# Optimization experiments

Measured on AMD Instinct MI355X. Metric: run time of the kernel, lower is better.

The kernel has to match this reference:

```python
import jax, jax.numpy as jnp
import numpy as np
import math

SUN = 9.0            # global SuN constant in the repo (sudoku N=9)
TB = 16              # t-block size for L1-score computation (bounds peak memory)


def quick_gelu(x):
    return x * jax.nn.sigmoid(1.702 * x)


def l1_scores(q, k):
    # q, k: (b, t, h, d)  ->  scores (b, h, t, s) = -sum_d |q[b,t,h,:] - k[b,s,h,:]|
    # Blocked over t so we never materialize the full (b,t,s,h,d) tensor.
    b, t, h, d = q.shape
    nb = t // TB
    qb = q.reshape(b, nb, TB, h, d).swapaxes(0, 1)  # (nb, b, TB, h, d)

    def blk(carry, qi):
        # qi: (b, TB, h, d); diff block: (b, TB, s, h, d) -> (b, TB, s, h)
        s = -jnp.sum(jnp.abs(qi[:, :, None, :, :] - k[:, None, :, :, :]), axis=-1)
        return carry, s

    _, out = jax.lax.scan(blk, None, qb)            # (nb, b, TB, s, h)
    out = out.transpose(1, 0, 2, 3, 4).reshape(b, t, t, h)  # (b, t, s, h)
    return out.transpose(0, 3, 1, 2)                # (b, h, t, s)


def setup_inputs() -> dict:
    key = jax.random.key(0)
    ks = jax.random.split(key, 5)
    b, t, d, h = 8, 512, 128, 8
    x = jax.random.normal(ks[0], (b, t, d), dtype=jnp.float32)
    msk = jax.random.uniform(ks[1], (1, h, t, t), dtype=jnp.float32)
    # LinearM(d_model, n_head*2*d_model): w is (outdim, indim+1), uniform*scl, bias col zeroed
    scl_qv = math.sqrt(6.0) / math.sqrt(d + h * 2 * d)
    wqv_w = jax.random.uniform(ks[2], (h * 2 * d, d + 1), dtype=jnp.float32) * scl_qv
    wqv_w = wqv_w.at[:, -1].set(0.0)
    # LinearNobias(d_model, n_head): w is (n_head, d_model); used directly as per-head k-gate
    scl_k = math.sqrt(6.0) / math.sqrt(d + h)
    wk_w = jax.random.uniform(ks[3], (h, d), dtype=jnp.float32) * scl_k
    # fanout = LinearM(d_model, d_model)
    scl_f = math.sqrt(6.0) / math.sqrt(2 * d)
    fanout_w = jax.random.uniform(ks[4], (d, d + 1), dtype=jnp.float32) * scl_f
    fanout_w = fanout_w.at[:, -1].set(0.0)
    return {"x": x, "msk": msk, "wqv_w": wqv_w, "wk_w": wk_w, "fanout_w": fanout_w}


def reference(x, msk, wqv_w, wk_w, fanout_w):
    b, t, d = x.shape
    h = wk_w.shape[0]
    # wqv: LinearM -> (b, t, h*2*d)
    y = jnp.einsum('oi,bti->bto', wqv_w[:, :-1], x) + wqv_w[:, -1]
    y = y.reshape(b, t, h, 2 * d)
    q, v = y[..., :d], y[..., d:]                      # each (b, t, h, d)
    # k = x expanded per head, gated elementwise by wk.w (per-head, per-dim gate)
    k = x[:, :, None, :] * wk_w[None, None, :, :]      # (b, t, h, d)
    # gv gate: all heads enabled (init_zeros=False) -> identity multiply on v
    a = l1_scores(q, k) / math.sqrt(d)                 # (b, h, t, s)
    a = jax.nn.softmax(a, axis=3) * msk                # mask AFTER softmax (as in source)
    # combine + sum over heads: einsum('bhts,bshd->bthd') then sum(dim=2 of bthd == h)
    bo = jnp.einsum('bhts,bshd->btd', a, v)            # (b, t, d)
    yo = quick_gelu(bo + SUN / 2.0) - SUN / 2.0
    yo = jnp.einsum('oi,bti->bto', fanout_w[:, :-1], yo) + fanout_w[:, -1]
    return x + yo
```

## Files before the change

### kernel.cpp

```cpp
#include <hip/hip_runtime.h>
#include <hip/hip_bf16.h>
#include <math.h>

#define BB 8
#define TT 512
#define DD 128
#define HH 8
#define OO 2048
#define WCOLS 129
#define SCALE 0.08838834764831845f
#define IT 16
#define SC2 64
#define NC (TT / SC2)
#define Q8SCL 32.0f
#define Q8OFF 128.0f
#define SCALE_Q8 (SCALE / Q8SCL)

typedef __attribute__((ext_vector_type(8))) short short8;
typedef __attribute__((ext_vector_type(4))) float floatx4;

static __device__ __forceinline__ float bf2f(__hip_bfloat16 v) { return __bfloat162float(v); }
static __device__ __forceinline__ float us2f(unsigned short u) {
  union { unsigned int i; float f; } cv; cv.i = ((unsigned int)u) << 16; return cv.f;
}
static __device__ __forceinline__ unsigned short f2us(float f) {
  union { float f; unsigned int i; } cv; cv.f = f;
  unsigned int lsb = (cv.i >> 16) & 1u;
  return (unsigned short)((cv.i + 0x7fffu + lsb) >> 16);
}
static __device__ __forceinline__ float ldin(const void* p, int i, int isf) {
  return isf ? ((const float*)p)[i] : bf2f(((const __hip_bfloat16*)p)[i]);
}
static __device__ __forceinline__ unsigned char quant8(float v) {
  float f = fminf(fmaxf(v * Q8SCL + Q8OFF, 0.0f), 255.0f);
  return (unsigned char)(f + 0.5f);
}
static __device__ __forceinline__ int detect_isf(const void* x) {
  const unsigned int* w = (const unsigned int*)x;
  int cnt = 0;
#pragma unroll
  for (int i = 0; i < 64; ++i) {
    float a = fabsf(us2f((unsigned short)(w[i] & 0xFFFFu)));
    cnt += (a > 0.05f && a < 8.0f) ? 1 : 0;
  }
  return (cnt < 32) ? 1 : 0;
}

#if __has_builtin(__builtin_amdgcn_sad_u8)
#define SAD8(a, b, c) __builtin_amdgcn_sad_u8((a), (b), (c))
#elif __has_builtin(__builtin_amdgcn_sad_u16)
static __device__ __forceinline__ unsigned int SAD8(unsigned int a, unsigned int b, unsigned int c) {
  unsigned int alo = a & 0x00FF00FFu, ahi = (a >> 8) & 0x00FF00FFu;
  unsigned int blo = b & 0x00FF00FFu, bhi = (b >> 8) & 0x00FF00FFu;
  c = __builtin_amdgcn_sad_u16(alo, blo, c);
  return __builtin_amdgcn_sad_u16(ahi, bhi, c);
}
#else
static __device__ __forceinline__ unsigned int SAD8(unsigned int a, unsigned int b, unsigned int c) {
#pragma unroll
  for (int i = 0; i < 4; ++i) {
    int d = (int)((a >> (8 * i)) & 0xFF) - (int)((b >> (8 * i)) & 0xFF);
    c += (unsigned int)(d < 0 ? -d : d);
  }
  return c;
}
#endif

__global__ void k_prep(const void* __restrict__ x,
                       const void* __restrict__ wqv,
                       const void* __restrict__ wk,
                       const void* __restrict__ fo,
                       float* __restrict__ qvb,
                       float* __restrict__ foT, float* __restrict__ fob,
                       float* __restrict__ wkf,
                       unsigned short* __restrict__ wqvb,
                       unsigned short* __restrict__ xb,
                       int* __restrict__ flg) {
  int isf = detect_isf(x);
  int stride = gridDim.x * blockDim.x;
  int idx = blockIdx.x * blockDim.x + threadIdx.x;
  if (idx == 0) *flg = isf;
  for (int i = idx; i < OO * DD; i += stride) {
    int o = i >> 7, ii = i & 127;
    wqvb[i] = f2us(ldin(wqv, o * WCOLS + ii, isf));
  }
  for (int o = idx; o < OO; o += stride) qvb[o] = ldin(wqv, o * WCOLS + DD, isf);
  for (int i = idx; i < DD * DD; i += stride) {
    int o = i & (DD - 1), ii = i >> 7;
    foT[i] = ldin(fo, o * WCOLS + ii, isf);
  }
  for (int o = idx; o < DD; o += stride) fob[o] = ldin(fo, o * WCOLS + DD, isf);
  for (int i = idx; i < HH * DD; i += stride) wkf[i] = ldin(wk, i, isf);
  {
    int n4 = BB * TT * DD / 4;
    for (int i4 = idx; i4 < n4; i4 += stride) {
      if (isf) {
        float4 f = ((const float4*)x)[i4];
        unsigned int lo = (unsigned int)f2us(f.x) | ((unsigned int)f2us(f.y) << 16);
        unsigned int hi = (unsigned int)f2us(f.z) | ((unsigned int)f2us(f.w) << 16);
        uint2 o2; o2.x = lo; o2.y = hi;
        ((uint2*)xb)[i4] = o2;
      } else {
        ((uint2*)xb)[i4] = ((const uint2*)x)[i4];
      }
    }
  }
}

__global__ __launch_bounds__(256) void k_qvm(const unsigned short* __restrict__ xb,
                                             const unsigned short* __restrict__ wqvb,
                                             const float* __restrict__ qvb,
                                             unsigned char* __restrict__ q2b,
                                             unsigned short* __restrict__ vt) {
  __shared__ __align__(16) unsigned short xs[32][136];
  __shared__ __align__(16) unsigned short vtile[128][40];
  __shared__ __align__(16) unsigned char qtile[32][144];
  int rb = blockIdx.x * 32;
  int cb = blockIdx.y * 256;
  int tid = threadIdx.x;
#pragma unroll
  for (int p = 0; p < 2; ++p) {
    int e = tid + p * 256;
    int row = e >> 4, c16 = e & 15;
    *(uint4*)&xs[row][c16 * 8] = *(const uint4*)&xb[(size_t)(rb + row) * DD + c16 * 8];
  }
  __syncthreads();
  int lane = tid & 63;
  int w = tid >> 6;
  int mI = lane & 15;
  int quad = lane >> 4;
  int cw = cb + w * 64;
  floatx4 acc[2][4];
#pragma unroll
  for (int rt = 0; rt < 2; ++rt)
#pragma unroll
    for (int ct = 0; ct < 4; ++ct) acc[rt][ct] = (floatx4){0.f, 0.f, 0.f, 0.f};
#pragma unroll
  for (int j = 0; j < 4; ++j) {
    short8 av[2], bv[4];
#pragma unroll
    for (int rt = 0; rt < 2; ++rt)
      av[rt] = *(const short8*)&xs[rt * 16 + mI][j * 32 + quad * 8];
#pragma unroll
    for (int ct = 0; ct < 4; ++ct)
      bv[ct] = *(const short8*)&wqvb[(size_t)(cw + ct * 16 + mI) * DD + j * 32 + quad * 8];
#pragma unroll
    for (int rt = 0; rt < 2; ++rt)
#pragma unroll
      for (int ct = 0; ct < 4; ++ct)
        acc[rt][ct] = __builtin_amdgcn_mfma_f32_16x16x32_bf16(av[rt], bv[ct], acc[rt][ct], 0, 0, 0);
  }
#pragma unroll
  for (int rt = 0; rt < 2; ++rt) {
#pragma unroll
    for (int ct = 0; ct < 4; ++ct) {
      int o = cw + ct * 16 + mI;
      float bias = qvb[o];
      int cc = o & 255;
#pragma unroll
      for (int reg = 0; reg < 4; ++reg) {
        int r = rb + rt * 16 + quad * 4 + reg;
        float val = acc[rt][ct][reg] + bias;
        if (cc < DD) qtile[r - rb][cc] = quant8(val);
        else         vtile[cc - DD][r - rb] = f2us(val);
      }
    }
  }
  __syncthreads();
  {
    int b = rb >> 9, t0 = rb & 511;
    int h = cb >> 8;
    {
      int row = tid >> 3, c16 = (tid & 7) * 16;
      unsigned char* qdst = q2b + ((size_t)(b * HH + h) * TT + t0 + row) * DD + c16;
      *(uint4*)qdst = *(const uint4*)&qtile[row][c16];
    }
    {
      int n = tid >> 1, half = tid & 1;
      unsigned short* dst = vt + (((size_t)(b * HH + h) * DD) + n) * TT + t0 + half * 16;
      uint4 a0 = *(const uint4*)&vtile[n][half * 16];
      uint4 a1 = *(const uint4*)&vtile[n][half * 16 + 8];
      *(uint4*)&dst[0] = a0;
      *(uint4*)&dst[8] = a1;
    }
  }
}

__global__ void k_k(const unsigned short* __restrict__ xb,
                    const float* __restrict__ wkf, unsigned char* __restrict__ ku8) {
  int idx = blockIdx.x * 256 + threadIdx.x;
  int d = idx & 127;
  int s = (idx >> 7) & 511;
  int h = (idx >> 16) & 7;
  int b = idx >> 19;
  float val = us2f(xb[(b * TT + s) * DD + d]) * wkf[h * DD + d];
  ku8[idx] = quant8(val);
}

static __device__ __forceinline__ void sad_chunk(const unsigned int (*__restrict__ kb)[36],
                                                 const unsigned int (*__restrict__ qp)[36],
                                                 int r0, int r1, int si, int rot,
                                                 float* __restrict__ r, int c) {
  unsigned int a00 = 0, a01 = 0, a10 = 0, a11 = 0;
  const unsigned int* k0r = &kb[2 * si][0];
  const unsigned int* k1r = &kb[2 * si + 1][0];
  const unsigned int* q0r = &qp[r0][0];
  const unsigned int* q1r = &qp[r1][0];
#pragma unroll
  for (int j8 = 0; j8 < 32; j8 += 8) {
    int i0 = (j8 + rot) & 31;
    int i1 = (j8 + rot + 4) & 31;
    uint4 qa0 = *(const uint4*)&q0r[i0];
    uint4 qa1 = *(const uint4*)&q0r[i1];
    uint4 qb0 = *(const uint4*)&q1r[i0];
    uint4 qb1 = *(const uint4*)&q1r[i1];
    uint4 ka0 = *(const uint4*)&k0r[i0];
    uint4 ka1 = *(const uint4*)&k0r[i1];
    uint4 kb0 = *(const uint4*)&k1r[i0];
    uint4 kb1 = *(const uint4*)&k1r[i1];
    a00 = SAD8(qa0.x, ka0.x, a00); a00 = SAD8(qa0.y, ka0.y, a00);
    a00 = SAD8(qa0.z, ka0.z, a00); a00 = SAD8(qa0.w, ka0.w, a00);
    a00 = SAD8(qa1.x, ka1.x, a00); a00 = SAD8(qa1.y, ka1.y, a00);
    a00 = SAD8(qa1.z, ka1.z, a00); a00 = SAD8(qa1.w, ka1.w, a00);
    a01 = SAD8(qa0.x, kb0.x, a01); a01 = SAD8(qa0.y, kb0.y, a01);
    a01 = SAD8(qa0.z, kb0.z, a01); a01 = SAD8(qa0.w, kb0.w, a01);
    a01 = SAD8(qa1.x, kb1.x, a01); a01 = SAD8(qa1.y, kb1.y, a01);
    a01 = SAD8(qa1.z, kb1.z, a01); a01 = SAD8(qa1.w, kb1.w, a01);
    a10 = SAD8(qb0.x, ka0.x, a10); a10 = SAD8(qb0.y, ka0.y, a10);
    a10 = SAD8(qb0.z, ka0.z, a10); a10 = SAD8(qb0.w, ka0.w, a10);
    a10 = SAD8(qb1.x, ka1.x, a10); a10 = SAD8(qb1.y, ka1.y, a10);
    a10 = SAD8(qb1.z, ka1.z, a10); a10 = SAD8(qb1.w, ka1.w, a10);
    a11 = SAD8(qb0.x, kb0.x, a11); a11 = SAD8(qb0.y, kb0.y, a11);
    a11 = SAD8(qb0.z, kb0.z, a11); a11 = SAD8(qb0.w, kb0.w, a11);
    a11 = SAD8(qb1.x, kb1.x, a11); a11 = SAD8(qb1.y, kb1.y, a11);
    a11 = SAD8(qb1.z, kb1.z, a11); a11 = SAD8(qb1.w, kb1.w, a11);
  }
  r[c * 2]          = -(float)a00 * SCALE_Q8;
  r[c * 2 + 1]      = -(float)a01 * SCALE_Q8;
  r[16 + c * 2]     = -(float)a10 * SCALE_Q8;
  r[16 + c * 2 + 1] = -(float)a11 * SCALE_Q8;
}

__global__ __launch_bounds__(256) void k_flash(const void* __restrict__ msk,
                                               const int* __restrict__ flag,
                                               const unsigned char* __restrict__ q2b,
                                               const unsigned char* __restrict__ ku8,
                                               const unsigned short* __restrict__ vt,
                                               unsigned short* __restrict__ yo8) {
  __shared__ __align__(16) unsigned char smem[2304 + 9216 + 16640];
  unsigned int (*qp)[36]  = (unsigned int (*)[36])smem;
  unsigned int (*kpA)[36] = (unsigned int (*)[36])(smem + 2304);
  unsigned int (*kpB)[36] = (unsigned int (*)[36])(smem + 11520);
  unsigned short (*ps)[TT + 8] = (unsigned short (*)[TT + 8])(smem + 11520);
  int isf = *flag;
  int bh = blockIdx.x;
  int h = bh & 7;
  int it0 = blockIdx.y * IT;
  int tid = threadIdx.x;

  const uint4* qrow = (const uint4*)(q2b + ((size_t)bh * TT + it0) * DD);
  if (tid < 128) {
    *(uint4*)&qp[tid >> 3][(tid & 7) * 4] = qrow[tid];
  }

  int ig2 = tid >> 5;
  int si = tid & 31;
  int r0 = ig2 * 2, r1 = r0 + 1;
  int rot = (si & 7) * 4;
  float r[32];

  const uint4* kc4 = (const uint4*)(ku8 + (size_t)bh * TT * DD);
  uint4 kreg[2];
#pragma unroll
  for (int p = 0; p < 2; ++p) kreg[p] = kc4[tid + p * 256];

#pragma unroll
  for (int cc = 0; cc < NC; cc += 2) {
#pragma unroll
    for (int p = 0; p < 2; ++p) {
      int e = tid + p * 256;
      *(uint4*)&kpA[e >> 3][(e & 7) * 4] = kreg[p];
    }
#pragma unroll
    for (int p = 0; p < 2; ++p)
      kreg[p] = kc4[(cc + 1) * 512 + tid + p * 256];
    __syncthreads();
    sad_chunk(kpA, qp, r0, r1, si, rot, r, cc);
#pragma unroll
    for (int p = 0; p < 2; ++p) {
      int e = tid + p * 256;
      *(uint4*)&kpB[e >> 3][(e & 7) * 4] = kreg[p];
    }
    if (cc + 2 < NC) {
#pragma unroll
      for (int p = 0; p < 2; ++p)
        kreg[p] = kc4[(cc + 2) * 512 + tid + p * 256];
    }
    __syncthreads();
    sad_chunk(kpB, qp, r0, r1, si, rot, r, cc + 1);
  }

  float m0 = -1e30f, m1 = -1e30f;
#pragma unroll
  for (int j = 0; j < 16; ++j) { m0 = fmaxf(m0, r[j]); m1 = fmaxf(m1, r[16 + j]); }
#pragma unroll
  for (int off = 16; off; off >>= 1) {
    m0 = fmaxf(m0, __shfl_xor(m0, off, 32));
    m1 = fmaxf(m1, __shfl_xor(m1, off, 32));
  }
  float s0 = 0.f, s1 = 0.f;
#pragma unroll
  for (int j = 0; j < 16; ++j) {
    r[j] = __expf(r[j] - m0);           s0 += r[j];
    r[16 + j] = __expf(r[16 + j] - m1); s1 += r[16 + j];
  }
#pragma unroll
  for (int off = 16; off; off >>= 1) {
    s0 += __shfl_xor(s0, off, 32);
    s1 += __shfl_xor(s1, off, 32);
  }
  float inv0 = 1.0f / s0, inv1 = 1.0f / s1;

  __syncthreads();

  int mb0 = (h * TT + it0 + r0) * TT;
  int mb1 = mb0 + TT;
#pragma unroll
  for (int c = 0; c < NC; ++c) {
    int s = c * SC2 + 2 * si;
    float p00 = r[c * 2]          * inv0 * ldin(msk, mb0 + s, isf);
    float p01 = r[c * 2 + 1]      * inv0 * ldin(msk, mb0 + s + 1, isf);
    float p10 = r[16 + c * 2]     * inv1 * ldin(msk, mb1 + s, isf);
    float p11 = r[16 + c * 2 + 1] * inv1 * ldin(msk, mb1 + s + 1, isf);
    *(unsigned int*)&ps[r0][s] = (unsigned int)f2us(p00) | ((unsigned int)f2us(p01) << 16);
    *(unsigned int*)&ps[r1][s] = (unsigned int)f2us(p10) | ((unsigned int)f2us(p11) << 16);
  }
  __syncthreads();

  {
    int lane = tid & 63;
    int w = tid >> 6;
    int mI = lane & 15;
    int quad = lane >> 4;
    int n0 = w * 32;
    floatx4 acc0 = {0.f, 0.f, 0.f, 0.f};
    floatx4 acc1 = {0.f, 0.f, 0.f, 0.f};
    const unsigned short* vb0 = vt + ((size_t)bh * DD + n0 + mI) * TT;
    const unsigned short* vb1 = vb0 + 16 * TT;
#pragma unroll
    for (int st = 0; st < 4; ++st) {
      short8 av[4], b0v[4], b1v[4];
#pragma unroll
      for (int j = 0; j < 4; ++j) {
        int krow = st * 128 + j * 32 + quad * 8;
        b0v[j] = *(const short8*)&vb0[krow];
        b1v[j] = *(const short8*)&vb1[krow];
        av[j]  = *(const short8*)&ps[mI][krow];
      }
#pragma unroll
      for (int j = 0; j < 4; ++j) {
        acc0 = __builtin_amdgcn_mfma_f32_16x16x32_bf16(av[j], b0v[j], acc0, 0, 0, 0);
        acc1 = __builtin_amdgcn_mfma_f32_16x16x32_bf16(av[j], b1v[j], acc1, 0, 0, 0);
      }
    }
    unsigned short* yb = yo8 + ((size_t)bh * TT + it0) * DD;
#pragma unroll
    for (int reg = 0; reg < 4; ++reg) {
      int row = quad * 4 + reg;
      yb[row * DD + n0 + mI]      = f2us(acc0[reg]);
      yb[row * DD + n0 + 16 + mI] = f2us(acc1[reg]);
    }
  }
}

__global__ __launch_bounds__(256) void k_fanout(const void* __restrict__ x,
                                                const int* __restrict__ flag,
                                                const unsigned short* __restrict__ yo8,
                                                const float* __restrict__ foT,
                                                const float* __restrict__ fob,
                                                void* __restrict__ outv) {
  __shared__ float ys[16][132];
  int isf = *flag;
  int m0 = blockIdx.x * 16;
  int tid = threadIdx.x;
  {
    int mr = tid >> 4;
    int i8 = (tid & 15) * 8;
    int r = m0 + mr;
    int bb = r >> 9, t = r & 511;
    size_t base = ((size_t)bb * HH * TT + t) * DD + i8;
    float s[8] = {0.f, 0.f, 0.f, 0.f, 0.f, 0.f, 0.f, 0.f};
#pragma unroll
    for (int hh = 0; hh < HH; ++hh) {
      short8 v = *(const short8*)&yo8[base + (size_t)hh * TT * DD];
#pragma unroll
      for (int j = 0; j < 8; ++j) s[j] += us2f((unsigned short)v[j]);
    }
#pragma unroll
    for (int j = 0; j < 8; ++j) {
      float z = s[j] + 4.5f;
      ys[mr][i8 + j] = z / (1.0f + __expf(-1.702f * z)) - 4.5f;
    }
  }
  __syncthreads();
  int ty = tid >> 5, tx = tid & 31;
  float acc[2][4] = {};
  for (int ii = 0; ii < 128; ++ii) {
    float4 w4 = *(const float4*)(foT + ii * DD + tx * 4);
    float y0 = ys[ty * 2 + 0][ii], y1 = ys[ty * 2 + 1][ii];
    acc[0][0] += y0 * w4.x; acc[0][1] += y0 * w4.y; acc[0][2] += y0 * w4.z; acc[0][3] += y0 * w4.w;
    acc[1][0] += y1 * w4.x; acc[1][1] += y1 * w4.y; acc[1][2] += y1 * w4.z; acc[1][3] += y1 * w4.w;
  }
#pragma unroll
  for (int rr = 0; rr < 2; ++rr) {
    int r = m0 + ty * 2 + rr;
#pragma unroll
    for (int c = 0; c < 4; ++c) {
      int o = tx * 4 + c;
      float val = acc[rr][c] + fob[o] + ldin(x, r * DD + o, isf);
      if (isf) ((float*)outv)[r * DD + o] = val;
      else     ((__hip_bfloat16*)outv)[r * DD + o] = __float2bfloat16(val);
    }
  }
}

extern "C" void kernel_launch(void* const* d_in, const int* in_sizes, int n_in,
                              void* d_out, int out_size, void* d_ws, size_t ws_size,
                              hipStream_t stream) {
  const void* x   = d_in[0];
  const void* msk = d_in[1];
  const void* wqv = d_in[2];
  const void* wk  = d_in[3];
  const void* fo  = d_in[4];

  float* qvb = (float*)d_ws;
  float* foT = qvb + 2048;
  float* fob = foT + 16384;
  float* wkf = fob + 128;
  int*   flg = (int*)(wkf + 1024);
  unsigned short* wqvb = (unsigned short*)(flg + 16);
  unsigned short* xb   = wqvb + 262144;
  unsigned char*  q2b  = (unsigned char*)(xb + 524288);
  unsigned char*  ku8  = q2b + 4194304;
  unsigned short* v2   = (unsigned short*)(ku8 + 4194304);
  unsigned short* vt   = v2 + 4194304;
  unsigned short* yo8  = v2;

  k_prep<<<256, 256, 0, stream>>>(x, wqv, wk, fo, qvb, foT, fob, wkf, wqvb, xb, flg);
  k_qvm<<<dim3(128, 8), 256, 0, stream>>>(xb, wqvb, qvb, q2b, vt);
  k_k<<<16384, 256, 0, stream>>>(xb, wkf, ku8);
  k_flash<<<dim3(64, 32), 256, 0, stream>>>(msk, flg, q2b, ku8, vt, yo8);
  k_fanout<<<256, 256, 0, stream>>>(x, flg, yo8, foT, fob, d_out);
}
```

Measured before the change: 184.3 us.

## Fuse key quantization into prep kernel and single-buffer K tiles in flash

```diff
diff --git a/kernel.cpp b/kernel.cpp
--- a/kernel.cpp
+++ b/kernel.cpp
@@ -72,9 +72,9 @@
                        const void* __restrict__ fo,
                        float* __restrict__ qvb,
                        float* __restrict__ foT, float* __restrict__ fob,
-                       float* __restrict__ wkf,
                        unsigned short* __restrict__ wqvb,
                        unsigned short* __restrict__ xb,
+                       unsigned char* __restrict__ ku8,
                        int* __restrict__ flg) {
   int isf = detect_isf(x);
   int stride = gridDim.x * blockDim.x;
@@ -90,18 +90,37 @@
     foT[i] = ldin(fo, o * WCOLS + ii, isf);
   }
   for (int o = idx; o < DD; o += stride) fob[o] = ldin(fo, o * WCOLS + DD, isf);
-  for (int i = idx; i < HH * DD; i += stride) wkf[i] = ldin(wk, i, isf);
   {
     int n4 = BB * TT * DD / 4;
     for (int i4 = idx; i4 < n4; i4 += stride) {
+      unsigned short xs4[4];
       if (isf) {
         float4 f = ((const float4*)x)[i4];
-        unsigned int lo = (unsigned int)f2us(f.x) | ((unsigned int)f2us(f.y) << 16);
-        unsigned int hi = (unsigned int)f2us(f.z) | ((unsigned int)f2us(f.w) << 16);
-        uint2 o2; o2.x = lo; o2.y = hi;
-        ((uint2*)xb)[i4] = o2;
+        xs4[0] = f2us(f.x); xs4[1] = f2us(f.y); xs4[2] = f2us(f.z); xs4[3] = f2us(f.w);
       } else {
-        ((uint2*)xb)[i4] = ((const uint2*)x)[i4];
+        uint2 raw = ((const uint2*)x)[i4];
+        xs4[0] = (unsigned short)(raw.x & 0xFFFFu); xs4[1] = (unsigned short)(raw.x >> 16);
+        xs4[2] = (unsigned short)(raw.y & 0xFFFFu); xs4[3] = (unsigned short)(raw.y >> 16);
+      }
+      uint2 o2;
+      o2.x = (unsigned int)xs4[0] | ((unsigned int)xs4[1] << 16);
+      o2.y = (unsigned int)xs4[2] | ((unsigned int)xs4[3] << 16);
+      ((uint2*)xb)[i4] = o2;
+      float xf[4];
+#pragma unroll
+      for (int j = 0; j < 4; ++j) xf[j] = us2f(xs4[j]);
+      int d0 = (i4 & 31) * 4;
+      int bs = i4 >> 5;
+      size_t kbase = ((size_t)(bs >> 9) * HH * TT + (size_t)(bs & 511)) * DD + d0;
+#pragma unroll
+      for (int hh = 0; hh < HH; ++hh) {
+        unsigned char kb0 = quant8(xf[0] * ldin(wk, hh * DD + d0 + 0, isf));
+        unsigned char kb1 = quant8(xf[1] * ldin(wk, hh * DD + d0 + 1, isf));
+        unsigned char kb2 = quant8(xf[2] * ldin(wk, hh * DD + d0 + 2, isf));
+        unsigned char kb3 = quant8(xf[3] * ldin(wk, hh * DD + d0 + 3, isf));
+        unsigned int wd = (unsigned int)kb0 | ((unsigned int)kb1 << 8) |
+                          ((unsigned int)kb2 << 16) | ((unsigned int)kb3 << 24);
+        *(unsigned int*)(ku8 + kbase + (size_t)hh * TT * DD) = wd;
       }
     }
   }
@@ -186,72 +205,15 @@
   }
 }
 
-__global__ void k_k(const unsigned short* __restrict__ xb,
-                    const float* __restrict__ wkf, unsigned char* __restrict__ ku8) {
-  int idx = blockIdx.x * 256 + threadIdx.x;
-  int d = idx & 127;
-  int s = (idx >> 7) & 511;
-  int h = (idx >> 16) & 7;
-  int b = idx >> 19;
-  float val = us2f(xb[(b * TT + s) * DD + d]) * wkf[h * DD + d];
-  ku8[idx] = quant8(val);
-}
-
-static __device__ __forceinline__ void sad_chunk(const unsigned int (*__restrict__ kb)[36],
-                                                 const unsigned int (*__restrict__ qp)[36],
-                                                 int r0, int r1, int si, int rot,
-                                                 float* __restrict__ r, int c) {
-  unsigned int a00 = 0, a01 = 0, a10 = 0, a11 = 0;
-  const unsigned int* k0r = &kb[2 * si][0];
-  const unsigned int* k1r = &kb[2 * si + 1][0];
-  const unsigned int* q0r = &qp[r0][0];
-  const unsigned int* q1r = &qp[r1][0];
-#pragma unroll
-  for (int j8 = 0; j8 < 32; j8 += 8) {
-    int i0 = (j8 + rot) & 31;
-    int i1 = (j8 + rot + 4) & 31;
-    uint4 qa0 = *(const uint4*)&q0r[i0];
-    uint4 qa1 = *(const uint4*)&q0r[i1];
-    uint4 qb0 = *(const uint4*)&q1r[i0];
-    uint4 qb1 = *(const uint4*)&q1r[i1];
-    uint4 ka0 = *(const uint4*)&k0r[i0];
-    uint4 ka1 = *(const uint4*)&k0r[i1];
-    uint4 kb0 = *(const uint4*)&k1r[i0];
-    uint4 kb1 = *(const uint4*)&k1r[i1];
-    a00 = SAD8(qa0.x, ka0.x, a00); a00 = SAD8(qa0.y, ka0.y, a00);
-    a00 = SAD8(qa0.z, ka0.z, a00); a00 = SAD8(qa0.w, ka0.w, a00);
-    a00 = SAD8(qa1.x, ka1.x, a00); a00 = SAD8(qa1.y, ka1.y, a00);
-    a00 = SAD8(qa1.z, ka1.z, a00); a00 = SAD8(qa1.w, ka1.w, a00);
-    a01 = SAD8(qa0.x, kb0.x, a01); a01 = SAD8(qa0.y, kb0.y, a01);
-    a01 = SAD8(qa0.z, kb0.z, a01); a01 = SAD8(qa0.w, kb0.w, a01);
-    a01 = SAD8(qa1.x, kb1.x, a01); a01 = SAD8(qa1.y, kb1.y, a01);
-    a01 = SAD8(qa1.z, kb1.z, a01); a01 = SAD8(qa1.w, kb1.w, a01);
-    a10 = SAD8(qb0.x, ka0.x, a10); a10 = SAD8(qb0.y, ka0.y, a10);
-    a10 = SAD8(qb0.z, ka0.z, a10); a10 = SAD8(qb0.w, ka0.w, a10);
-    a10 = SAD8(qb1.x, ka1.x, a10); a10 = SAD8(qb1.y, ka1.y, a10);
-    a10 = SAD8(qb1.z, ka1.z, a10); a10 = SAD8(qb1.w, ka1.w, a10);
-    a11 = SAD8(qb0.x, kb0.x, a11); a11 = SAD8(qb0.y, kb0.y, a11);
-    a11 = SAD8(qb0.z, kb0.z, a11); a11 = SAD8(qb0.w, kb0.w, a11);
-    a11 = SAD8(qb1.x, kb1.x, a11); a11 = SAD8(qb1.y, kb1.y, a11);
-    a11 = SAD8(qb1.z, kb1.z, a11); a11 = SAD8(qb1.w, kb1.w, a11);
-  }
-  r[c * 2]          = -(float)a00 * SCALE_Q8;
-  r[c * 2 + 1]      = -(float)a01 * SCALE_Q8;
-  r[16 + c * 2]     = -(float)a10 * SCALE_Q8;
-  r[16 + c * 2 + 1] = -(float)a11 * SCALE_Q8;
-}
-
 __global__ __launch_bounds__(256) void k_flash(const void* __restrict__ msk,
                                                const int* __restrict__ flag,
                                                const unsigned char* __restrict__ q2b,
                                                const unsigned char* __restrict__ ku8,
                                                const unsigned short* __restrict__ vt,
                                                unsigned short* __restrict__ yo8) {
-  __shared__ __align__(16) unsigned char smem[2304 + 9216 + 16640];
-  unsigned int (*qp)[36]  = (unsigned int (*)[36])smem;
-  unsigned int (*kpA)[36] = (unsigned int (*)[36])(smem + 2304);
-  unsigned int (*kpB)[36] = (unsigned int (*)[36])(smem + 11520);
-  unsigned short (*ps)[TT + 8] = (unsigned short (*)[TT + 8])(smem + 11520);
+  __shared__ __align__(16) unsigned int qp[IT][36];
+  __shared__ __align__(16) unsigned int kp[SC2][36];
+  __shared__ __align__(16) unsigned short ps[IT][TT + 8];
   int isf = *flag;
   int bh = blockIdx.x;
   int h = bh & 7;
@@ -275,29 +237,57 @@
   for (int p = 0; p < 2; ++p) kreg[p] = kc4[tid + p * 256];
 
 #pragma unroll
-  for (int cc = 0; cc < NC; cc += 2) {
+  for (int c = 0; c < NC; ++c) {
+    __syncthreads();
 #pragma unroll
     for (int p = 0; p < 2; ++p) {
       int e = tid + p * 256;
-      *(uint4*)&kpA[e >> 3][(e & 7) * 4] = kreg[p];
-    }
-#pragma unroll
-    for (int p = 0; p < 2; ++p)
-      kreg[p] = kc4[(cc + 1) * 512 + tid + p * 256];
+      *(uint4*)&kp[e >> 3][(e & 7) * 4] = kreg[p];
+    }
+    if (c < NC - 1) {
+#pragma unroll
+      for (int p = 0; p < 2; ++p)
+        kreg[p] = kc4[(c + 1) * 512 + tid + p * 256];
+    }
     __syncthreads();
-    sad_chunk(kpA, qp, r0, r1, si, rot, r, cc);
-#pragma unroll
-    for (int p = 0; p < 2; ++p) {
-      int e = tid + p * 256;
-      *(uint4*)&kpB[e >> 3][(e & 7) * 4] = kreg[p];
-    }
-    if (cc + 2 < NC) {
-#pragma unroll
-      for (int p = 0; p < 2; ++p)
-        kreg[p] = kc4[(cc + 2) * 512 + tid + p * 256];
-    }
-    __syncthreads();
-    sad_chunk(kpB, qp, r0, r1, si, rot, r, cc + 1);
+    unsigned int a00 = 0, a01 = 0, a10 = 0, a11 = 0;
+    const unsigned int* k0r = &kp[2 * si][0];
+    const unsigned int* k1r = &kp[2 * si + 1][0];
+    const unsigned int* q0r = &qp[r0][0];
+    const unsigned int* q1r = &qp[r1][0];
+#pragma unroll
+    for (int j8 = 0; j8 < 32; j8 += 8) {
+      int i0 = (j8 + rot) & 31;
+      int i1 = (j8 + rot + 4) & 31;
+      uint4 qa0 = *(const uint4*)&q0r[i0];
+      uint4 qa1 = *(const uint4*)&q0r[i1];
+      uint4 qb0 = *(const uint4*)&q1r[i0];
+      uint4 qb1 = *(const uint4*)&q1r[i1];
+      uint4 ka0 = *(const uint4*)&k0r[i0];
+      uint4 ka1 = *(const uint4*)&k0r[i1];
+      uint4 kb0 = *(const uint4*)&k1r[i0];
+      uint4 kb1 = *(const uint4*)&k1r[i1];
+      a00 = SAD8(qa0.x, ka0.x, a00); a00 = SAD8(qa0.y, ka0.y, a00);
+      a00 = SAD8(qa0.z, ka0.z, a00); a00 = SAD8(qa0.w, ka0.w, a00);
+      a00 = SAD8(qa1.x, ka1.x, a00); a00 = SAD8(qa1.y, ka1.y, a00);
+      a00 = SAD8(qa1.z, ka1.z, a00); a00 = SAD8(qa1.w, ka1.w, a00);
+      a01 = SAD8(qa0.x, kb0.x, a01); a01 = SAD8(qa0.y, kb0.y, a01);
+      a01 = SAD8(qa0.z, kb0.z, a01); a01 = SAD8(qa0.w, kb0.w, a01);
+      a01 = SAD8(qa1.x, kb1.x, a01); a01 = SAD8(qa1.y, kb1.y, a01);
+      a01 = SAD8(qa1.z, kb1.z, a01); a01 = SAD8(qa1.w, kb1.w, a01);
+      a10 = SAD8(qb0.x, ka0.x, a10); a10 = SAD8(qb0.y, ka0.y, a10);
+      a10 = SAD8(qb0.z, ka0.z, a10); a10 = SAD8(qb0.w, ka0.w, a10);
+      a10 = SAD8(qb1.x, ka1.x, a10); a10 = SAD8(qb1.y, ka1.y, a10);
+      a10 = SAD8(qb1.z, ka1.z, a10); a10 = SAD8(qb1.w, ka1.w, a10);
+      a11 = SAD8(qb0.x, kb0.x, a11); a11 = SAD8(qb0.y, kb0.y, a11);
+      a11 = SAD8(qb0.z, kb0.z, a11); a11 = SAD8(qb0.w, kb0.w, a11);
+      a11 = SAD8(qb1.x, kb1.x, a11); a11 = SAD8(qb1.y, kb1.y, a11);
+      a11 = SAD8(qb1.z, kb1.z, a11); a11 = SAD8(qb1.w, kb1.w, a11);
+    }
+    r[c * 2]          = -(float)a00 * SCALE_Q8;
+    r[c * 2 + 1]      = -(float)a01 * SCALE_Q8;
+    r[16 + c * 2]     = -(float)a10 * SCALE_Q8;
+    r[16 + c * 2 + 1] = -(float)a11 * SCALE_Q8;
   }
 
   float m0 = -1e30f, m1 = -1e30f;
@@ -320,8 +310,6 @@
     s1 += __shfl_xor(s1, off, 32);
   }
   float inv0 = 1.0f / s0, inv1 = 1.0f / s1;
-
-  __syncthreads();
 
   int mb0 = (h * TT + it0 + r0) * TT;
   int mb1 = mb0 + TT;
@@ -446,9 +434,8 @@
   unsigned short* vt   = v2 + 4194304;
   unsigned short* yo8  = v2;
 
-  k_prep<<<256, 256, 0, stream>>>(x, wqv, wk, fo, qvb, foT, fob, wkf, wqvb, xb, flg);
+  k_prep<<<256, 256, 0, stream>>>(x, wqv, wk, fo, qvb, foT, fob, wqvb, xb, ku8, flg);
   k_qvm<<<dim3(128, 8), 256, 0, stream>>>(xb, wqvb, qvb, q2b, vt);
-  k_k<<<16384, 256, 0, stream>>>(xb, wkf, ku8);
   k_flash<<<dim3(64, 32), 256, 0, stream>>>(msk, flg, q2b, ku8, vt, yo8);
   k_fanout<<<256, 256, 0, stream>>>(x, flg, yo8, foT, fob, d_out);
 }
```

Result: faster. 177.3 us (-3.8%).
